# Kernel tuning notes

Hardware: AMD Instinct MI355X
Metric: run time of the kernel (lower is better)

## Reference

```python
import jax, jax.numpy as jnp
import numpy as np

HD = 512          # head_dim
ROPE = 64         # qk_rope_head_dim
RATIO = 4         # compress_ratio (overlap=True, coff=2)
EPS = 1e-6


def setup_inputs() -> dict:
    key = jax.random.key(0)
    ks = jax.random.split(key, 6)
    B, S, H = 4, 4096, 4096
    C = S // RATIO
    return {
        "x": jax.random.normal(ks[0], (B, S, H), dtype=jnp.float32),
        "cos": jax.random.uniform(ks[1], (B, C, ROPE // 2), dtype=jnp.float32),
        "sin": jax.random.uniform(ks[2], (B, C, ROPE // 2), dtype=jnp.float32),
        "W_kv": jax.random.normal(ks[3], (2 * HD, H), dtype=jnp.float32) * 0.02,
        "W_gate": jax.random.normal(ks[4], (2 * HD, H), dtype=jnp.float32) * 0.02,
        "ape": jax.random.normal(ks[5], (RATIO, 2 * HD), dtype=jnp.float32),
        "norm_w": jnp.ones((HD,), dtype=jnp.float32),
    }


def reference(x, cos, sin, W_kv, W_gate, ape, norm_w):
    B, S, H = x.shape
    C = S // RATIO  # compressed_len (S divisible by RATIO)
    # projections + sigmoid gate
    kv = jnp.einsum("bsh,oh->bso", x, W_kv)
    kv = kv * jax.nn.sigmoid(jnp.einsum("bsh,oh->bso", x, W_gate))
    # split into chunks of RATIO tokens: [B, C, RATIO, 2*HD]
    kvr = kv.reshape(B, C, RATIO, 2 * HD)
    main = kvr[..., :HD]          # main half of projection
    ov = kvr[..., HD:]            # overlap half
    # learned pooling weights (softmax over the RATIO (+overlap) axis)
    ape_comb = jnp.concatenate([ape[:, :HD], ape[:, HD:]], axis=0)  # [2*RATIO, HD]
    w8 = jax.nn.softmax(ape_comb, axis=0)     # weights for i > 0 (main||overlap)
    w0 = jax.nn.softmax(ape[:, :HD], axis=0)  # weights for i == 0 (no overlap)
    out = jnp.einsum("bcrd,rd->bcd", main, w8[:RATIO])
    out = out.at[:, 1:].add(jnp.einsum("bcrd,rd->bcd", ov[:, :-1], w8[RATIO:]))
    out = out.at[:, 0].set(jnp.einsum("brd,rd->bd", main[:, 0], w0))
    # RMSNorm over head_dim
    var = jnp.mean(out * out, axis=-1, keepdims=True)
    out = out * jax.lax.rsqrt(var + EPS) * norm_w
    # partial interleaved rotary on last ROPE dims
    x1 = out[..., : HD - ROPE]
    x2 = out[..., HD - ROPE :]
    x2e, x2o = x2[..., 0::2], x2[..., 1::2]           # [B, C, ROPE//2]
    re = x2e * cos - x2o * sin
    ro = x2e * sin + x2o * cos
    rot = jnp.stack([re, ro], axis=-1).reshape(B, C, ROPE)
    return jnp.concatenate([x1, rot], axis=-1)
```

## Files before the change

kernel.cpp:

```cpp
#include <hip/hip_runtime.h>


typedef __attribute__((ext_vector_type(8))) __bf16 bf16x8;
typedef __attribute__((ext_vector_type(4))) float f32x4;

__device__ __forceinline__ void gld16(const void* g, void* l) {
    __builtin_amdgcn_global_load_lds(
        (const __attribute__((address_space(1))) void*)g,
        (__attribute__((address_space(3))) void*)l, 16, 0, 0);
}
__device__ __forceinline__ unsigned short bf16rn(float f) {
    unsigned int u = __float_as_uint(f);
    u += 0x7FFF + ((u >> 16) & 1);
    return (unsigned short)(u >> 16);
}
__device__ __forceinline__ float bf16tof(unsigned short h) {
    return __uint_as_float(((unsigned int)h) << 16);
}

__global__ void convert_x_kernel(const float4* __restrict__ src,
                                 ushort4* __restrict__ hi,
                                 ushort4* __restrict__ lo) {
    const int i = blockIdx.x * 256 + threadIdx.x;
    const float4 v = src[i];
    ushort4 h, l;
    h.x = bf16rn(v.x); l.x = bf16rn(v.x - bf16tof(h.x));
    h.y = bf16rn(v.y); l.y = bf16rn(v.y - bf16tof(h.y));
    h.z = bf16rn(v.z); l.z = bf16rn(v.z - bf16tof(h.z));
    h.w = bf16rn(v.w); l.w = bf16rn(v.w - bf16tof(h.w));
    hi[i] = h; lo[i] = l;
}

__global__ void convert_w_kernel(const float* __restrict__ Wkv,
                                 const float* __restrict__ Wgate,
                                 ushort4* __restrict__ hi,
                                 ushort4* __restrict__ lo) {
    const int i = blockIdx.x * 256 + threadIdx.x;
    const size_t e = (size_t)i * 4;
    const int r = (int)(e >> 12);
    const int col = (int)(e & 4095);
    const int grp = r >> 5, wi = r & 31;
    const int srow = grp * 16 + (wi & 15);
    const float* srcrow = (wi < 16) ? (Wkv + ((size_t)srow << 12))
                                    : (Wgate + ((size_t)srow << 12));
    const float4 v = *(const float4*)(srcrow + col);
    ushort4 h, l;
    h.x = bf16rn(v.x); l.x = bf16rn(v.x - bf16tof(h.x));
    h.y = bf16rn(v.y); l.y = bf16rn(v.y - bf16tof(h.y));
    h.z = bf16rn(v.z); l.z = bf16rn(v.z - bf16tof(h.z));
    h.w = bf16rn(v.w); l.w = bf16rn(v.w - bf16tof(h.w));
    hi[i] = h; lo[i] = l;
}

__global__ void softmax_kernel(const float* __restrict__ ape,
                               float* __restrict__ w8,
                               float* __restrict__ w0) {
    const int d = threadIdx.x;
    float v[8];
#pragma unroll
    for (int r = 0; r < 4; ++r) v[r] = ape[r * 1024 + d];
#pragma unroll
    for (int r = 0; r < 4; ++r) v[4 + r] = ape[r * 1024 + 512 + d];
    float mx = v[0];
#pragma unroll
    for (int i = 1; i < 8; ++i) mx = fmaxf(mx, v[i]);
    float e[8], s = 0.f;
#pragma unroll
    for (int i = 0; i < 8; ++i) { e[i] = expf(v[i] - mx); s += e[i]; }
    const float inv = 1.f / s;
#pragma unroll
    for (int i = 0; i < 8; ++i) w8[i * 512 + d] = e[i] * inv;
    float mx4 = fmaxf(fmaxf(v[0], v[1]), fmaxf(v[2], v[3]));
    float e4[4], s4 = 0.f;
#pragma unroll
    for (int i = 0; i < 4; ++i) { e4[i] = expf(v[i] - mx4); s4 += e4[i]; }
    const float inv4 = 1.f / s4;
#pragma unroll
    for (int i = 0; i < 4; ++i) w0[i * 512 + d] = e4[i] * inv4;
}

#define BAR() __builtin_amdgcn_s_barrier()
#define WAIT_LGKM0() asm volatile("s_waitcnt lgkmcnt(0)" ::: "memory")
#define WAIT_VM(n) asm volatile("s_waitcnt vmcnt(" #n ")" ::: "memory")

#define STAGE(g, h, bu) do {                                                   \
    const int seg_ = (g) >> 6;                                                 \
    const size_t kc_ = (size_t)(((g) & 63) * 64);                              \
    const unsigned short* bp_; size_t b0_, b1_; unsigned int lb_;              \
    if ((h) < 2) { bp_ = (seg_ == 1) ? Xlo : Xhi; b0_ = baseA0; b1_ = baseA1; lb_ = 0u; } \
    else         { bp_ = (seg_ == 2) ? Wlo : Whi; b0_ = baseB0; b1_ = baseB1; lb_ = 32768u; } \
    const size_t hof_ = ((h) & 1) ? (size_t)524288 : 0;   \
    const unsigned int ld_ = (unsigned)(bu) * 65536u + lb_ + (((h) & 1) ? 16384u : 0u); \
    gld16(bp_ + b0_ + hof_ + kc_, lds + ld_ + off0);                           \
    gld16(bp_ + b1_ + hof_ + kc_, lds + ld_ + off1);                           \
} while (0)

#define LDA(bu, mh) do {                                                       \
    const char* p_ = aRow + (bu) * 65536u + (mh) * 8192u;                      \
    _Pragma("unroll") for (int mi = 0; mi < 4; ++mi) {                         \
        ra[mi][0] = *(const bf16x8*)(p_ + mi * 2048 + koff0);                  \
        ra[mi][1] = *(const bf16x8*)(p_ + mi * 2048 + (koff0 ^ 64)); }         \
} while (0)

#define LDB(bu, nh, rb) do {                                                   \
    const char* p_ = bRow + (bu) * 65536u + (nh) * 4096u;                      \
    _Pragma("unroll") for (int ni = 0; ni < 2; ++ni) {                         \
        rb[ni][0] = *(const bf16x8*)(p_ + ni * 2048 + koff0);                  \
        rb[ni][1] = *(const bf16x8*)(p_ + ni * 2048 + (koff0 ^ 64)); }         \
} while (0)

#define MM(mh, nh, rb) do {                                                    \
    __builtin_amdgcn_s_setprio(1);                                             \
    _Pragma("unroll") for (int mi = 0; mi < 4; ++mi)                           \
    _Pragma("unroll") for (int ni = 0; ni < 2; ++ni)                           \
    _Pragma("unroll") for (int kk = 0; kk < 2; ++kk)                           \
        acc[(mh) * 4 + mi][(nh) * 2 + ni] =                                    \
            __builtin_amdgcn_mfma_f32_16x16x32_bf16(                           \
                ra[mi][kk], rb[ni][kk], acc[(mh) * 4 + mi][(nh) * 2 + ni], 0, 0, 0); \
    __builtin_amdgcn_s_setprio(0);                                             \
} while (0)

template <int SPLITBUF>
__global__ __launch_bounds__(512, 2) void gemm8_kernel(
    const unsigned short* __restrict__ Xhi, const unsigned short* __restrict__ Xlo,
    const unsigned short* __restrict__ Whi, const unsigned short* __restrict__ Wlo,
    float* __restrict__ C) {
    extern __shared__ char lds[];
    const int t = threadIdx.x;
    const int lane = t & 63;
    const int w = t >> 6;
    const int wm = (w >> 2) * 128;
    const int wn = (w & 3) * 64;

    const int sw = (blockIdx.x & 7) * 32 + (blockIdx.x >> 3);
    const int z = sw & 1;
    const int bn = (sw >> 1) & 7;
    const int bm = sw >> 4;

    const unsigned int off0 = t * 16u;
    const unsigned int off1 = off0 + 8192u;
    const unsigned int r0 = off0 >> 7, r1 = off1 >> 7;
    const unsigned int sc0 = ((off0 >> 4) & 7) ^ (r0 & 7);
    const unsigned int sc1 = ((off1 >> 4) & 7) ^ (r1 & 7);
    const size_t baseA0 = (size_t)(bm * 256 + r0) * 4096 + sc0 * 8;
    const size_t baseA1 = (size_t)(bm * 256 + r1) * 4096 + sc1 * 8;
    const size_t baseB0 = (size_t)(bn * 256 + r0) * 4096 + sc0 * 8;
    const size_t baseB1 = (size_t)(bn * 256 + r1) * 4096 + sc1 * 8;

    const unsigned int koff0 = (((lane >> 4) * 16u) ^ ((lane & 7) << 4));
    const char* aRow = lds + (unsigned)(wm + (lane & 15)) * 128u;
    const char* bRow = lds + 32768u + (unsigned)(wn + (lane & 15)) * 128u;

    f32x4 acc[8][4];
    const f32x4 zero = {0.f, 0.f, 0.f, 0.f};
#pragma unroll
    for (int mi = 0; mi < 8; ++mi)
#pragma unroll
        for (int nj = 0; nj < 4; ++nj) acc[mi][nj] = zero;

    bf16x8 ra[4][2], rb0[2][2], rb1[2][2];

    const int g00 = z * 96;
    STAGE(g00, 0, 0); STAGE(g00, 1, 0); STAGE(g00, 2, 0); STAGE(g00, 3, 0);
    STAGE(g00 + 1, 0, 1);
    WAIT_VM(2); BAR();

    for (int i = 0; i < 48; ++i) {
        const int ga = g00 + 2 * i;
        const int gb = ga + 1;
        const bool nl = (i < 47);
        LDA(0, 0); LDB(0, 0, rb0);
        STAGE(gb, 1, 1);
        BAR(); WAIT_LGKM0();
        MM(0, 0, rb0);
        BAR();
        LDB(0, 1, rb1);
        STAGE(gb, 2, 1);
        BAR(); WAIT_LGKM0();
        MM(0, 1, rb1);
        BAR();
        LDA(0, 1);
        STAGE(gb, 3, 1);
        BAR(); WAIT_LGKM0();
        MM(1, 1, rb1);
        BAR();
        if (nl) { STAGE(ga + 2, 0, 0); }
        MM(1, 0, rb0);
        if (nl) { WAIT_VM(2); } else { WAIT_VM(0); }
        BAR();
        LDA(1, 0); LDB(1, 0, rb0);
        if (nl) { STAGE(ga + 2, 1, 0); }
        BAR(); WAIT_LGKM0();
        MM(0, 0, rb0);
        BAR();
        LDB(1, 1, rb1);
        if (nl) { STAGE(ga + 2, 2, 0); }
        BAR(); WAIT_LGKM0();
        MM(0, 1, rb1);
        BAR();
        LDA(1, 1);
        if (nl) { STAGE(ga + 2, 3, 0); }
        BAR(); WAIT_LGKM0();
        MM(1, 1, rb1);
        BAR();
        if (nl) {
            STAGE(ga + 3, 0, 1);
            MM(1, 0, rb0);
            WAIT_VM(2); BAR();
        } else {
            MM(1, 0, rb0);
        }
    }

    const int c0 = bn * 256 + wn + (lane & 15);
    const int r0e = bm * 256 + wm + (lane >> 4) * 4;
    if (SPLITBUF) {
        float* Co = C + (size_t)z * 8388608;
#pragma unroll
        for (int mi = 0; mi < 8; ++mi)
#pragma unroll
            for (int nj = 0; nj < 4; ++nj) {
                float* cp = Co + (size_t)(r0e + mi * 16) * 2048 + (c0 + nj * 16);
#pragma unroll
                for (int ii = 0; ii < 4; ++ii) cp[(size_t)ii * 2048] = acc[mi][nj][ii];
            }
    } else {
#pragma unroll
        for (int mi = 0; mi < 8; ++mi)
#pragma unroll
            for (int nj = 0; nj < 4; ++nj) {
                float* cp = C + (size_t)(r0e + mi * 16) * 2048 + (c0 + nj * 16);
#pragma unroll
                for (int ii = 0; ii < 4; ++ii) atomicAdd(cp + (size_t)ii * 2048, acc[mi][nj][ii]);
            }
    }
}

template <int SPLIT>
__global__ void combine2_kernel(const float* __restrict__ C0,
                                const float* __restrict__ w8,
                                const float* __restrict__ w0,
                                const float* __restrict__ cosb,
                                const float* __restrict__ sinb,
                                const float* __restrict__ normw,
                                float* __restrict__ outb) {
    const int c = blockIdx.x;
    const int t = threadIdx.x;
    const int d = t * 2;
    const int jm = ((d >> 4) * 32) + (d & 15);
    float o0 = 0.f, o1 = 0.f;

    const float* rowp = C0 + (size_t)c * (4 * 2048);
    const float* wsel = (c == 0) ? w0 : w8;
#pragma unroll
    for (int r = 0; r < 4; ++r) {
        const float* rp = rowp + r * 2048;
        float2 kv = *(const float2*)(rp + jm);
        float2 gt = *(const float2*)(rp + jm + 16);
        if (SPLIT) {
            const float2 kv1 = *(const float2*)(rp + 8388608 + jm);
            const float2 gt1 = *(const float2*)(rp + 8388608 + jm + 16);
            kv.x += kv1.x; kv.y += kv1.y; gt.x += gt1.x; gt.y += gt1.y;
        }
        o0 += (kv.x / (1.f + expf(-gt.x))) * wsel[r * 512 + d];
        o1 += (kv.y / (1.f + expf(-gt.y))) * wsel[r * 512 + d + 1];
    }
    if (c > 0) {
        const float* prow = C0 + (size_t)(c - 1) * (4 * 2048) + 1024;
#pragma unroll
        for (int r = 0; r < 4; ++r) {
            const float* rp = prow + r * 2048;
            float2 kv = *(const float2*)(rp + jm);
            float2 gt = *(const float2*)(rp + jm + 16);
            if (SPLIT) {
                const float2 kv1 = *(const float2*)(rp + 8388608 + jm);
                const float2 gt1 = *(const float2*)(rp + 8388608 + jm + 16);
                kv.x += kv1.x; kv.y += kv1.y; gt.x += gt1.x; gt.y += gt1.y;
            }
            o0 += (kv.x / (1.f + expf(-gt.x))) * w8[(4 + r) * 512 + d];
            o1 += (kv.y / (1.f + expf(-gt.y))) * w8[(4 + r) * 512 + d + 1];
        }
    }

    float p = o0 * o0 + o1 * o1;
#pragma unroll
    for (int off = 32; off > 0; off >>= 1) p += __shfl_down(p, off, 64);
    __shared__ float red[4];
    if ((t & 63) == 0) red[t >> 6] = p;
    __syncthreads();
    const float sc = rsqrtf((red[0] + red[1] + red[2] + red[3]) * (1.f / 512.f) + 1e-6f);
    o0 *= sc * normw[d];
    o1 *= sc * normw[d + 1];

    float2 res;
    if (d < 448) {
        res.x = o0; res.y = o1;
    } else {
        const int j = (d - 448) >> 1;
        const float cv = cosb[c * 32 + j];
        const float sv = sinb[c * 32 + j];
        res.x = o0 * cv - o1 * sv;
        res.y = o0 * sv + o1 * cv;
    }
    *(float2*)(outb + (size_t)c * 512 + d) = res;
}

extern "C" void kernel_launch(void* const* d_in, const int* in_sizes, int n_in,
                              void* d_out, int out_size, void* d_ws, size_t ws_size,
                              hipStream_t stream) {
    const float* x     = (const float*)d_in[0];
    const float* cosp  = (const float*)d_in[1];
    const float* sinp  = (const float*)d_in[2];
    const float* Wkv   = (const float*)d_in[3];
    const float* Wgate = (const float*)d_in[4];
    const float* ape   = (const float*)d_in[5];
    const float* normw = (const float*)d_in[6];
    float* outp = (float*)d_out;

    char* wsb = (char*)d_ws;
    const size_t MB = 1024 * 1024;
    unsigned short* Xhi = (unsigned short*)(wsb);
    unsigned short* Xlo = (unsigned short*)(wsb + 32 * MB);
    unsigned short* Whi = (unsigned short*)(wsb + 64 * MB);
    unsigned short* Wlo = (unsigned short*)(wsb + 80 * MB);
    float* Cz = (float*)(wsb + 96 * MB);

    const bool split = (ws_size >= 160 * MB + 32768);
    char* tail = wsb + (split ? 160 * MB : 128 * MB);
    float* W8 = (float*)tail;
    float* W0 = (float*)(tail + 16384);

    (void)hipFuncSetAttribute((const void*)gemm8_kernel<1>,
                              hipFuncAttributeMaxDynamicSharedMemorySize, 131072);
    (void)hipFuncSetAttribute((const void*)gemm8_kernel<0>,
                              hipFuncAttributeMaxDynamicSharedMemorySize, 131072);

    convert_w_kernel<<<8192, 256, 0, stream>>>(Wkv, Wgate, (ushort4*)Whi, (ushort4*)Wlo);
    softmax_kernel<<<1, 512, 0, stream>>>(ape, W8, W0);

    for (int b = 0; b < 4; ++b) {
        convert_x_kernel<<<16384, 256, 0, stream>>>(
            (const float4*)(x + (size_t)b * 16777216), (ushort4*)Xhi, (ushort4*)Xlo);
        if (split) {
            gemm8_kernel<1><<<256, 512, 131072, stream>>>(Xhi, Xlo, Whi, Wlo, Cz);
            combine2_kernel<1><<<1024, 256, 0, stream>>>(
                Cz, W8, W0, cosp + (size_t)b * 32768, sinp + (size_t)b * 32768,
                normw, outp + (size_t)b * 524288);
        } else {
            hipMemsetAsync(Cz, 0, 32 * MB, stream);
            gemm8_kernel<0><<<256, 512, 131072, stream>>>(Xhi, Xlo, Whi, Wlo, Cz);
            combine2_kernel<0><<<1024, 256, 0, stream>>>(
                Cz, W8, W0, cosp + (size_t)b * 32768, sinp + (size_t)b * 32768,
                normw, outp + (size_t)b * 524288);
        }
    }
}
```

Measured before the change: 1.117 ms.

## Restage GEMM prefetch in paired chunks and widen bf16 split conversion to 8 elements

The GEMM main loop now issues its global-to-LDS stages two chunks at a time, earlier in the iteration. The whole next half-tile is preloaded before the loop, and the vmcnt waits are relaxed from 2 to 8 outstanding loads, so memory traffic overlaps longer with the MFMA work. Separately, the x and W hi/lo bf16 conversion kernels now handle 8 elements per thread, with two float4 loads and 16-byte stores, and launch half as many blocks. The new schedule changes which LDS buffers are in flight when, which risks read-after-write hazards if the wait counts don't line up with the issue order.

```diff
diff --git a/kernel.cpp b/kernel.cpp
--- a/kernel.cpp
+++ b/kernel.cpp
@@ -3,6 +3,7 @@
 
 typedef __attribute__((ext_vector_type(8))) __bf16 bf16x8;
 typedef __attribute__((ext_vector_type(4))) float f32x4;
+typedef __attribute__((ext_vector_type(8))) unsigned short u16x8;
 
 __device__ __forceinline__ void gld16(const void* g, void* l) {
     __builtin_amdgcn_global_load_lds(
@@ -18,38 +19,45 @@
     return __uint_as_float(((unsigned int)h) << 16);
 }
 
-__global__ void convert_x_kernel(const float4* __restrict__ src,
-                                 ushort4* __restrict__ hi,
-                                 ushort4* __restrict__ lo) {
-    const int i = blockIdx.x * 256 + threadIdx.x;
-    const float4 v = src[i];
-    ushort4 h, l;
-    h.x = bf16rn(v.x); l.x = bf16rn(v.x - bf16tof(h.x));
-    h.y = bf16rn(v.y); l.y = bf16rn(v.y - bf16tof(h.y));
-    h.z = bf16rn(v.z); l.z = bf16rn(v.z - bf16tof(h.z));
-    h.w = bf16rn(v.w); l.w = bf16rn(v.w - bf16tof(h.w));
-    hi[i] = h; lo[i] = l;
+__global__ void convert_x_kernel(const float* __restrict__ src,
+                                 unsigned short* __restrict__ hi,
+                                 unsigned short* __restrict__ lo) {
+    const size_t i = ((size_t)blockIdx.x * 256 + threadIdx.x) * 8;
+    const float4 v0 = *(const float4*)(src + i);
+    const float4 v1 = *(const float4*)(src + i + 4);
+    float v[8] = {v0.x, v0.y, v0.z, v0.w, v1.x, v1.y, v1.z, v1.w};
+    u16x8 h, l;
+#pragma unroll
+    for (int j = 0; j < 8; ++j) {
+        h[j] = bf16rn(v[j]);
+        l[j] = bf16rn(v[j] - bf16tof(h[j]));
+    }
+    *(u16x8*)(hi + i) = h;
+    *(u16x8*)(lo + i) = l;
 }
 
 __global__ void convert_w_kernel(const float* __restrict__ Wkv,
                                  const float* __restrict__ Wgate,
-                                 ushort4* __restrict__ hi,
-                                 ushort4* __restrict__ lo) {
-    const int i = blockIdx.x * 256 + threadIdx.x;
-    const size_t e = (size_t)i * 4;
-    const int r = (int)(e >> 12);
-    const int col = (int)(e & 4095);
+                                 unsigned short* __restrict__ hi,
+                                 unsigned short* __restrict__ lo) {
+    const size_t i = ((size_t)blockIdx.x * 256 + threadIdx.x) * 8;
+    const int r = (int)(i >> 12);
+    const int col = (int)(i & 4095);
     const int grp = r >> 5, wi = r & 31;
     const int srow = grp * 16 + (wi & 15);
     const float* srcrow = (wi < 16) ? (Wkv + ((size_t)srow << 12))
                                     : (Wgate + ((size_t)srow << 12));
-    const float4 v = *(const float4*)(srcrow + col);
-    ushort4 h, l;
-    h.x = bf16rn(v.x); l.x = bf16rn(v.x - bf16tof(h.x));
-    h.y = bf16rn(v.y); l.y = bf16rn(v.y - bf16tof(h.y));
-    h.z = bf16rn(v.z); l.z = bf16rn(v.z - bf16tof(h.z));
-    h.w = bf16rn(v.w); l.w = bf16rn(v.w - bf16tof(h.w));
-    hi[i] = h; lo[i] = l;
+    const float4 v0 = *(const float4*)(srcrow + col);
+    const float4 v1 = *(const float4*)(srcrow + col + 4);
+    float v[8] = {v0.x, v0.y, v0.z, v0.w, v1.x, v1.y, v1.z, v1.w};
+    u16x8 h, l;
+#pragma unroll
+    for (int j = 0; j < 8; ++j) {
+        h[j] = bf16rn(v[j]);
+        l[j] = bf16rn(v[j] - bf16tof(h[j]));
+    }
+    *(u16x8*)(hi + i) = h;
+    *(u16x8*)(lo + i) = l;
 }
 
 __global__ void softmax_kernel(const float* __restrict__ ape,
@@ -162,51 +170,46 @@
 
     const int g00 = z * 96;
     STAGE(g00, 0, 0); STAGE(g00, 1, 0); STAGE(g00, 2, 0); STAGE(g00, 3, 0);
-    STAGE(g00 + 1, 0, 1);
-    WAIT_VM(2); BAR();
+    STAGE(g00 + 1, 0, 1); STAGE(g00 + 1, 1, 1); STAGE(g00 + 1, 2, 1); STAGE(g00 + 1, 3, 1);
+    WAIT_VM(8); BAR();
 
     for (int i = 0; i < 48; ++i) {
         const int ga = g00 + 2 * i;
-        const int gb = ga + 1;
         const bool nl = (i < 47);
         LDA(0, 0); LDB(0, 0, rb0);
-        STAGE(gb, 1, 1);
         BAR(); WAIT_LGKM0();
         MM(0, 0, rb0);
         BAR();
         LDB(0, 1, rb1);
-        STAGE(gb, 2, 1);
         BAR(); WAIT_LGKM0();
         MM(0, 1, rb1);
         BAR();
+        if (nl) { STAGE(ga + 2, 2, 0); STAGE(ga + 2, 3, 0); }
         LDA(0, 1);
-        STAGE(gb, 3, 1);
         BAR(); WAIT_LGKM0();
         MM(1, 1, rb1);
         BAR();
-        if (nl) { STAGE(ga + 2, 0, 0); }
+        if (nl) { STAGE(ga + 2, 0, 0); STAGE(ga + 2, 1, 0); }
         MM(1, 0, rb0);
-        if (nl) { WAIT_VM(2); } else { WAIT_VM(0); }
+        if (nl) { WAIT_VM(8); } else { WAIT_VM(0); }
         BAR();
         LDA(1, 0); LDB(1, 0, rb0);
-        if (nl) { STAGE(ga + 2, 1, 0); }
         BAR(); WAIT_LGKM0();
         MM(0, 0, rb0);
         BAR();
         LDB(1, 1, rb1);
-        if (nl) { STAGE(ga + 2, 2, 0); }
         BAR(); WAIT_LGKM0();
         MM(0, 1, rb1);
         BAR();
+        if (nl) { STAGE(ga + 3, 2, 1); STAGE(ga + 3, 3, 1); }
         LDA(1, 1);
-        if (nl) { STAGE(ga + 2, 3, 0); }
         BAR(); WAIT_LGKM0();
         MM(1, 1, rb1);
         BAR();
         if (nl) {
-            STAGE(ga + 3, 0, 1);
+            STAGE(ga + 3, 0, 1); STAGE(ga + 3, 1, 1);
             MM(1, 0, rb0);
-            WAIT_VM(2); BAR();
+            WAIT_VM(8); BAR();
         } else {
             MM(1, 0, rb0);
         }
@@ -335,12 +338,12 @@
     (void)hipFuncSetAttribute((const void*)gemm8_kernel<0>,
                               hipFuncAttributeMaxDynamicSharedMemorySize, 131072);
 
-    convert_w_kernel<<<8192, 256, 0, stream>>>(Wkv, Wgate, (ushort4*)Whi, (ushort4*)Wlo);
+    convert_w_kernel<<<4096, 256, 0, stream>>>(Wkv, Wgate, Whi, Wlo);
     softmax_kernel<<<1, 512, 0, stream>>>(ape, W8, W0);
 
     for (int b = 0; b < 4; ++b) {
-        convert_x_kernel<<<16384, 256, 0, stream>>>(
-            (const float4*)(x + (size_t)b * 16777216), (ushort4*)Xhi, (ushort4*)Xlo);
+        convert_x_kernel<<<8192, 256, 0, stream>>>(
+            x + (size_t)b * 16777216, Xhi, Xlo);
         if (split) {
             gemm8_kernel<1><<<256, 512, 131072, stream>>>(Xhi, Xlo, Whi, Wlo, Cz);
             combine2_kernel<1><<<1024, 256, 0, stream>>>(
```

Result: no change. 1.109 ms (-0.7%).
